# Performance work log

Measured on AMD Instinct MI355X. Metric: run time of the kernel, lower is better.

Reference implementation:

```python
import jax, jax.numpy as jnp
import numpy as np

N_QUBITS = 10
N_LAYERS = 4
DIM = 2 ** N_QUBITS  # 1024 statevector entries

# Z-expectation sign table: signs[d, q] = +1 if bit q of basis state d is 0 else -1
_bits = (np.arange(DIM)[:, None] >> (N_QUBITS - 1 - np.arange(N_QUBITS))) & 1
Z_SIGNS = jnp.asarray(1.0 - 2.0 * _bits, dtype=jnp.float32)  # [DIM, N_QUBITS]


def _apply_1q(state, mat, q):
    """Apply a 2x2 gate on qubit q. state: [B, DIM]; mat: [2,2] or [B,2,2]."""
    left, right = 2 ** q, 2 ** (N_QUBITS - q - 1)
    s = state.reshape(-1, left, 2, right)
    if mat.ndim == 3:
        s = jnp.einsum('bij,bljr->blir', mat, s)
    else:
        s = jnp.einsum('ij,bljr->blir', mat, s)
    return s.reshape(-1, DIM)


def _cnot_adj(state, q):
    """CNOT with control q, target q+1 (adjacent wires)."""
    left, right = 2 ** q, 2 ** (N_QUBITS - q - 2)
    s = state.reshape(-1, left, 2, 2, right)
    s = jnp.stack([s[:, :, 0], s[:, :, 1, ::-1]], axis=2)  # flip target where control=1
    return s.reshape(-1, DIM)


def _cnot_wrap(state):
    """CNOT with control = last qubit, target = qubit 0 (ring closure)."""
    s = state.reshape(-1, 2, 2 ** (N_QUBITS - 2), 2)  # [B, target, mid, control]
    s = jnp.stack([s[..., 0], s[:, ::-1, :, 1]], axis=-1)
    return s.reshape(-1, DIM)


def _circuit(x, weights):
    B = x.shape[0]
    state = jnp.zeros((B, DIM), jnp.complex64).at[:, 0].set(1.0)  # |0...0>

    # RX angle embedding (batch-dependent gates)
    c = jnp.cos(0.5 * x).astype(jnp.complex64)           # [B, n]
    s = (-1j) * jnp.sin(0.5 * x).astype(jnp.complex64)   # [B, n]
    for q in range(N_QUBITS):
        mat = jnp.stack([jnp.stack([c[:, q], s[:, q]], -1),
                         jnp.stack([s[:, q], c[:, q]], -1)], -2)  # [B,2,2]
        state = _apply_1q(state, mat, q)

    # BasicEntanglerLayers: per-qubit RY (shared weights) + CNOT ring
    w = weights.reshape(N_LAYERS, N_QUBITS)
    ch = jnp.cos(0.5 * w).astype(jnp.complex64)
    sh = jnp.sin(0.5 * w).astype(jnp.complex64)
    for l in range(N_LAYERS):
        for q in range(N_QUBITS):
            mat = jnp.stack([jnp.stack([ch[l, q], -sh[l, q]], -1),
                             jnp.stack([sh[l, q], ch[l, q]], -1)], -2)  # [2,2]
            state = _apply_1q(state, mat, q)
        for q in range(N_QUBITS - 1):
            state = _cnot_adj(state, q)
        state = _cnot_wrap(state)

    probs = state.real ** 2 + state.imag ** 2  # [B, DIM]
    return probs @ Z_SIGNS                     # [B, N_QUBITS] PauliZ expectations


def setup_inputs() -> dict:
    key = jax.random.key(0)
    k1, k2 = jax.random.split(key)
    x = jax.random.normal(k1, (2048, N_QUBITS), dtype=jnp.float32)
    weights = jax.random.normal(k2, (N_LAYERS * N_QUBITS,), dtype=jnp.float32)
    return {"x": x, "weights": weights}


def reference(x, weights):
    # Equivalent of: torch.stack([qnode(x[i], weights) for i in range(B)])
    # but fully batched over the statevector.
    return _circuit(x, weights)
```

## Files before the change

### kernel.cpp

```cpp
#include <hip/hip_runtime.h>

#define NQ 10
#define NL 4


template<int CTRL>
__device__ __forceinline__ float dppf(float v) {
    const int i = __float_as_int(v);
    const int r = __builtin_amdgcn_update_dpp(i, i, CTRL, 0xF, 0xF, false);
    return __int_as_float(r);
}
template<int OFF>
__device__ __forceinline__ float swzf(float v) {
    return __int_as_float(__builtin_amdgcn_ds_swizzle(__float_as_int(v), OFF));
}
__device__ __forceinline__ float bpermf(int addr4, float v) {
    return __int_as_float(__builtin_amdgcn_ds_bpermute(addr4, __float_as_int(v)));
}
__device__ __forceinline__ float rdlane(float v, int l) {
    return __int_as_float(__builtin_amdgcn_readlane(__float_as_int(v), l));
}

__global__ __launch_bounds__(256) void qnn_kernel(const float* __restrict__ x,
                                                  const float* __restrict__ w,
                                                  float* __restrict__ out,
                                                  int B) {
    const int lane = threadIdx.x & 63;
    const int b = blockIdx.x * 4 + (threadIdx.x >> 6);
    if (b >= B) return;

    float cxv = 1.f, sxv = 0.f, cwv = 1.f, swv = 0.f;
    if (lane < NQ) {
        const float a = 0.5f * x[b * NQ + lane];
        cxv = cosf(a); sxv = sinf(a);
    }
    if (lane < NL * NQ) {
        const float a = 0.5f * w[lane];
        cwv = cosf(a); swv = sinf(a);
    }

    float cq[NQ], sq[NQ];
#pragma unroll
    for (int q = 0; q < NQ; ++q) { cq[q] = rdlane(cxv, q); sq[q] = rdlane(sxv, q); }

    float ml = 1.f;
#pragma unroll
    for (int p = 0; p < 6; ++p) {
        ml *= ((lane >> p) & 1) ? sq[9 - p] : cq[9 - p];
    }
    const int kl = __popc(lane);
    const float cph = (kl & 1) ? 0.f : ((kl & 2) ? -1.f : 1.f);
    const float sph = (kl & 1) ? ((kl & 2) ? 1.f : -1.f) : 0.f;

    float m01[4], m23[4];
#pragma unroll
    for (int j = 0; j < 4; ++j) {
        m01[j] = ((j & 1) ? sq[3] : cq[3]) * ((j & 2) ? sq[2] : cq[2]);
        m23[j] = ((j & 1) ? sq[1] : cq[1]) * ((j & 2) ? sq[0] : cq[0]);
    }

    float2 v[16];
#pragma unroll
    for (int r = 0; r < 16; ++r) {
        const float M = ml * m01[r & 3] * m23[r >> 2];
        const int kr = ((r & 1) + ((r >> 1) & 1) + ((r >> 2) & 1) + ((r >> 3) & 1)) & 3;
        float re, im;
        if      (kr == 0) { re = cph;  im = sph;  }
        else if (kr == 1) { re = sph;  im = -cph; }
        else if (kr == 2) { re = -cph; im = -sph; }
        else              { re = -sph; im = cph;  }
        v[r] = make_float2(M * re, M * im);
    }

    int t = lane;
    t ^= ((t >> 1) & 1) << 0;
    t ^= ((t >> 2) & 1) << 1;
    t ^= ((t >> 3) & 1) << 2;
    t ^= ((t >> 4) & 1) << 3;
    t ^= ((t >> 5) & 1) << 4;
    const int ga4 = t << 2;
    const int gb4 = (t ^ 32) << 2;
    const int a32 = (lane ^ 32) << 2;
    const bool wrapctl = (lane & 1);

#pragma unroll
    for (int l = 0; l < NL; ++l) {
#pragma unroll
        for (int q = 0; q < 4; ++q) {
            const float c = rdlane(cwv, l * NQ + q);
            const float s = rdlane(swv, l * NQ + q);
            const int m = 1 << (3 - q);
#pragma unroll
            for (int r = 0; r < 16; ++r) {
                if (!(r & m)) {
                    const int r1 = r | m;
                    const float2 a0 = v[r], a1 = v[r1];
                    v[r]  = make_float2(c * a0.x - s * a1.x, c * a0.y - s * a1.y);
                    v[r1] = make_float2(s * a0.x + c * a1.x, s * a0.y + c * a1.y);
                }
            }
        }
        {
            const float c = rdlane(cwv, l * NQ + 4);
            const float s = rdlane(swv, l * NQ + 4);
            const float ss = (lane & 32) ? s : -s;
#pragma unroll
            for (int r = 0; r < 16; ++r) {
                const float ox = bpermf(a32, v[r].x);
                const float oy = bpermf(a32, v[r].y);
                v[r].x = fmaf(c, v[r].x, ss * ox);
                v[r].y = fmaf(c, v[r].y, ss * oy);
            }
        }
        {
            const float c = rdlane(cwv, l * NQ + 5);
            const float s = rdlane(swv, l * NQ + 5);
            const float ss = (lane & 16) ? s : -s;
#pragma unroll
            for (int r = 0; r < 16; ++r) {
                const float ox = swzf<0x401F>(v[r].x);
                const float oy = swzf<0x401F>(v[r].y);
                v[r].x = fmaf(c, v[r].x, ss * ox);
                v[r].y = fmaf(c, v[r].y, ss * oy);
            }
        }
        {
            const float c = rdlane(cwv, l * NQ + 6);
            const float s = rdlane(swv, l * NQ + 6);
            const float ss = (lane & 8) ? s : -s;
#pragma unroll
            for (int r = 0; r < 16; ++r) {
                const float ox = dppf<0x128>(v[r].x);
                const float oy = dppf<0x128>(v[r].y);
                v[r].x = fmaf(c, v[r].x, ss * ox);
                v[r].y = fmaf(c, v[r].y, ss * oy);
            }
        }
        {
            const float c = rdlane(cwv, l * NQ + 7);
            const float s = rdlane(swv, l * NQ + 7);
            const float ss = (lane & 4) ? s : -s;
#pragma unroll
            for (int r = 0; r < 16; ++r) {
                const float ox = swzf<0x101F>(v[r].x);
                const float oy = swzf<0x101F>(v[r].y);
                v[r].x = fmaf(c, v[r].x, ss * ox);
                v[r].y = fmaf(c, v[r].y, ss * oy);
            }
        }
        {
            const float c = rdlane(cwv, l * NQ + 8);
            const float s = rdlane(swv, l * NQ + 8);
            const float ss = (lane & 2) ? s : -s;
#pragma unroll
            for (int r = 0; r < 16; ++r) {
                const float ox = dppf<0x4E>(v[r].x);
                const float oy = dppf<0x4E>(v[r].y);
                v[r].x = fmaf(c, v[r].x, ss * ox);
                v[r].y = fmaf(c, v[r].y, ss * oy);
            }
        }
        {
            const float c = rdlane(cwv, l * NQ + 9);
            const float s = rdlane(swv, l * NQ + 9);
            const float ss = (lane & 1) ? s : -s;
#pragma unroll
            for (int r = 0; r < 16; ++r) {
                const float ox = dppf<0xB1>(v[r].x);
                const float oy = dppf<0xB1>(v[r].y);
                v[r].x = fmaf(c, v[r].x, ss * ox);
                v[r].y = fmaf(c, v[r].y, ss * oy);
            }
        }

        { float2 tmp;
          tmp = v[8];  v[8]  = v[12]; v[12] = tmp;
          tmp = v[9];  v[9]  = v[13]; v[13] = tmp;
          tmp = v[10]; v[10] = v[14]; v[14] = tmp;
          tmp = v[11]; v[11] = v[15]; v[15] = tmp; }
        { float2 tmp;
          tmp = v[4];  v[4]  = v[6];  v[6]  = tmp;
          tmp = v[5];  v[5]  = v[7];  v[7]  = tmp;
          tmp = v[12]; v[12] = v[14]; v[14] = tmp;
          tmp = v[13]; v[13] = v[15]; v[15] = tmp; }
        { float2 tmp;
          tmp = v[2];  v[2]  = v[3];  v[3]  = tmp;
          tmp = v[6];  v[6]  = v[7];  v[7]  = tmp;
          tmp = v[10]; v[10] = v[11]; v[11] = tmp;
          tmp = v[14]; v[14] = v[15]; v[15] = tmp; }
#pragma unroll
        for (int r = 0; r < 16; ++r) {
            const int a4 = (r & 1) ? gb4 : ga4;
            v[r].x = bpermf(a4, v[r].x);
            v[r].y = bpermf(a4, v[r].y);
        }
#pragma unroll
        for (int r = 0; r < 8; ++r) {
            const float2 a = v[r], c2 = v[r + 8];
            v[r]     = wrapctl ? c2 : a;
            v[r + 8] = wrapctl ? a : c2;
        }
    }

    float p[16];
    float T = 0.f;
#pragma unroll
    for (int r = 0; r < 16; ++r) {
        p[r] = v[r].x * v[r].x + v[r].y * v[r].y;
        T += p[r];
    }
    float S0 = 0.f, S1 = 0.f, S2 = 0.f, S3 = 0.f;
#pragma unroll
    for (int r = 0; r < 16; ++r) {
        S0 += (r & 8) ? -p[r] : p[r];
        S1 += (r & 4) ? -p[r] : p[r];
        S2 += (r & 2) ? -p[r] : p[r];
        S3 += (r & 1) ? -p[r] : p[r];
    }
    float acc[NQ];
    acc[0] = S0; acc[1] = S1; acc[2] = S2; acc[3] = S3;
#pragma unroll
    for (int q = 4; q < NQ; ++q) {
        acc[q] = ((lane >> (9 - q)) & 1) ? -T : T;
    }

#pragma unroll
    for (int q = 0; q < NQ; ++q) {
        float a = acc[q];
        a += bpermf(a32, a);
        a += swzf<0x401F>(a);
        a += dppf<0x128>(a);
        a += swzf<0x101F>(a);
        a += dppf<0x4E>(a);
        a += dppf<0xB1>(a);
        acc[q] = a;
    }
    if (lane == 0) {
#pragma unroll
        for (int q = 0; q < NQ; ++q) out[b * NQ + q] = acc[q];
    }
}

extern "C" void kernel_launch(void* const* d_in, const int* in_sizes, int n_in,
                              void* d_out, int out_size, void* d_ws, size_t ws_size,
                              hipStream_t stream) {
    const float* x = (const float*)d_in[0];
    const float* w = (const float*)d_in[1];
    float* out = (float*)d_out;
    const int B = in_sizes[0] / NQ;
    qnn_kernel<<<(B + 3) / 4, 256, 0, stream>>>(x, w, out, B);
}
```

Before: 71.47 us.

## Fold first entangler layer into product-state init and absorb final CNOT ring into readout

After: 66.75 us. 1.07x faster.

```diff
diff --git a/kernel.cpp b/kernel.cpp
--- a/kernel.cpp
+++ b/kernel.cpp
@@ -1,8 +1,9 @@
 #include <hip/hip_runtime.h>
 
 #define NQ 10
-#define NL 4
-
+
+
+typedef float v2f __attribute__((ext_vector_type(2)));
 
 template<int CTRL>
 __device__ __forceinline__ float dppf(float v) {
@@ -19,6 +20,13 @@
 }
 __device__ __forceinline__ float rdlane(float v, int l) {
     return __int_as_float(__builtin_amdgcn_readlane(__float_as_int(v), l));
+}
+__device__ __forceinline__ v2f splat(float a) { v2f r; r.x = a; r.y = a; return r; }
+__device__ __forceinline__ v2f cmul(v2f a, v2f b) {
+    v2f r;
+    r.x = a.x * b.x - a.y * b.y;
+    r.y = a.x * b.y + a.y * b.x;
+    return r;
 }
 
 __global__ __launch_bounds__(256) void qnn_kernel(const float* __restrict__ x,
@@ -34,43 +42,38 @@
         const float a = 0.5f * x[b * NQ + lane];
         cxv = cosf(a); sxv = sinf(a);
     }
-    if (lane < NL * NQ) {
+    if (lane < 4 * NQ) {
         const float a = 0.5f * w[lane];
         cwv = cosf(a); swv = sinf(a);
     }
 
-    float cq[NQ], sq[NQ];
-#pragma unroll
-    for (int q = 0; q < NQ; ++q) { cq[q] = rdlane(cxv, q); sq[q] = rdlane(sxv, q); }
-
-    float ml = 1.f;
-#pragma unroll
-    for (int p = 0; p < 6; ++p) {
-        ml *= ((lane >> p) & 1) ? sq[9 - p] : cq[9 - p];
-    }
-    const int kl = __popc(lane);
-    const float cph = (kl & 1) ? 0.f : ((kl & 2) ? -1.f : 1.f);
-    const float sph = (kl & 1) ? ((kl & 2) ? 1.f : -1.f) : 0.f;
-
-    float m01[4], m23[4];
+    v2f u0[NQ], u1[NQ];
+#pragma unroll
+    for (int q = 0; q < NQ; ++q) {
+        const float c  = rdlane(cxv, q), s  = rdlane(sxv, q);
+        const float ch = rdlane(cwv, q), sh = rdlane(swv, q);
+        u0[q].x = ch * c;  u0[q].y = sh * s;
+        u1[q].x = sh * c;  u1[q].y = -ch * s;
+    }
+
+    v2f ml = (lane & 1) ? u1[9] : u0[9];
+#pragma unroll
+    for (int p = 1; p < 6; ++p) {
+        const v2f f = ((lane >> p) & 1) ? u1[9 - p] : u0[9 - p];
+        ml = cmul(ml, f);
+    }
+    v2f m01[4], m23[4], tml[4];
 #pragma unroll
     for (int j = 0; j < 4; ++j) {
-        m01[j] = ((j & 1) ? sq[3] : cq[3]) * ((j & 2) ? sq[2] : cq[2]);
-        m23[j] = ((j & 1) ? sq[1] : cq[1]) * ((j & 2) ? sq[0] : cq[0]);
-    }
-
-    float2 v[16];
-#pragma unroll
-    for (int r = 0; r < 16; ++r) {
-        const float M = ml * m01[r & 3] * m23[r >> 2];
-        const int kr = ((r & 1) + ((r >> 1) & 1) + ((r >> 2) & 1) + ((r >> 3) & 1)) & 3;
-        float re, im;
-        if      (kr == 0) { re = cph;  im = sph;  }
-        else if (kr == 1) { re = sph;  im = -cph; }
-        else if (kr == 2) { re = -cph; im = -sph; }
-        else              { re = -sph; im = cph;  }
-        v[r] = make_float2(M * re, M * im);
-    }
+        m01[j] = cmul((j & 1) ? u1[3] : u0[3], (j & 2) ? u1[2] : u0[2]);
+        m23[j] = cmul((j & 1) ? u1[1] : u0[1], (j & 2) ? u1[0] : u0[0]);
+    }
+#pragma unroll
+    for (int j = 0; j < 4; ++j) tml[j] = cmul(ml, m01[j]);
+
+    v2f v[16];
+#pragma unroll
+    for (int r = 0; r < 16; ++r) v[r] = cmul(tml[r & 3], m23[r >> 2]);
 
     int t = lane;
     t ^= ((t >> 1) & 1) << 0;
@@ -84,106 +87,18 @@
     const bool wrapctl = (lane & 1);
 
 #pragma unroll
-    for (int l = 0; l < NL; ++l) {
-#pragma unroll
-        for (int q = 0; q < 4; ++q) {
-            const float c = rdlane(cwv, l * NQ + q);
-            const float s = rdlane(swv, l * NQ + q);
-            const int m = 1 << (3 - q);
-#pragma unroll
-            for (int r = 0; r < 16; ++r) {
-                if (!(r & m)) {
-                    const int r1 = r | m;
-                    const float2 a0 = v[r], a1 = v[r1];
-                    v[r]  = make_float2(c * a0.x - s * a1.x, c * a0.y - s * a1.y);
-                    v[r1] = make_float2(s * a0.x + c * a1.x, s * a0.y + c * a1.y);
-                }
-            }
-        }
-        {
-            const float c = rdlane(cwv, l * NQ + 4);
-            const float s = rdlane(swv, l * NQ + 4);
-            const float ss = (lane & 32) ? s : -s;
-#pragma unroll
-            for (int r = 0; r < 16; ++r) {
-                const float ox = bpermf(a32, v[r].x);
-                const float oy = bpermf(a32, v[r].y);
-                v[r].x = fmaf(c, v[r].x, ss * ox);
-                v[r].y = fmaf(c, v[r].y, ss * oy);
-            }
-        }
-        {
-            const float c = rdlane(cwv, l * NQ + 5);
-            const float s = rdlane(swv, l * NQ + 5);
-            const float ss = (lane & 16) ? s : -s;
-#pragma unroll
-            for (int r = 0; r < 16; ++r) {
-                const float ox = swzf<0x401F>(v[r].x);
-                const float oy = swzf<0x401F>(v[r].y);
-                v[r].x = fmaf(c, v[r].x, ss * ox);
-                v[r].y = fmaf(c, v[r].y, ss * oy);
-            }
-        }
-        {
-            const float c = rdlane(cwv, l * NQ + 6);
-            const float s = rdlane(swv, l * NQ + 6);
-            const float ss = (lane & 8) ? s : -s;
-#pragma unroll
-            for (int r = 0; r < 16; ++r) {
-                const float ox = dppf<0x128>(v[r].x);
-                const float oy = dppf<0x128>(v[r].y);
-                v[r].x = fmaf(c, v[r].x, ss * ox);
-                v[r].y = fmaf(c, v[r].y, ss * oy);
-            }
-        }
-        {
-            const float c = rdlane(cwv, l * NQ + 7);
-            const float s = rdlane(swv, l * NQ + 7);
-            const float ss = (lane & 4) ? s : -s;
-#pragma unroll
-            for (int r = 0; r < 16; ++r) {
-                const float ox = swzf<0x101F>(v[r].x);
-                const float oy = swzf<0x101F>(v[r].y);
-                v[r].x = fmaf(c, v[r].x, ss * ox);
-                v[r].y = fmaf(c, v[r].y, ss * oy);
-            }
-        }
-        {
-            const float c = rdlane(cwv, l * NQ + 8);
-            const float s = rdlane(swv, l * NQ + 8);
-            const float ss = (lane & 2) ? s : -s;
-#pragma unroll
-            for (int r = 0; r < 16; ++r) {
-                const float ox = dppf<0x4E>(v[r].x);
-                const float oy = dppf<0x4E>(v[r].y);
-                v[r].x = fmaf(c, v[r].x, ss * ox);
-                v[r].y = fmaf(c, v[r].y, ss * oy);
-            }
-        }
-        {
-            const float c = rdlane(cwv, l * NQ + 9);
-            const float s = rdlane(swv, l * NQ + 9);
-            const float ss = (lane & 1) ? s : -s;
-#pragma unroll
-            for (int r = 0; r < 16; ++r) {
-                const float ox = dppf<0xB1>(v[r].x);
-                const float oy = dppf<0xB1>(v[r].y);
-                v[r].x = fmaf(c, v[r].x, ss * ox);
-                v[r].y = fmaf(c, v[r].y, ss * oy);
-            }
-        }
-
-        { float2 tmp;
+    for (int l = 0; l < 3; ++l) {
+        { v2f tmp;
           tmp = v[8];  v[8]  = v[12]; v[12] = tmp;
           tmp = v[9];  v[9]  = v[13]; v[13] = tmp;
           tmp = v[10]; v[10] = v[14]; v[14] = tmp;
           tmp = v[11]; v[11] = v[15]; v[15] = tmp; }
-        { float2 tmp;
+        { v2f tmp;
           tmp = v[4];  v[4]  = v[6];  v[6]  = tmp;
           tmp = v[5];  v[5]  = v[7];  v[7]  = tmp;
           tmp = v[12]; v[12] = v[14]; v[14] = tmp;
           tmp = v[13]; v[13] = v[15]; v[15] = tmp; }
-        { float2 tmp;
+        { v2f tmp;
           tmp = v[2];  v[2]  = v[3];  v[3]  = tmp;
           tmp = v[6];  v[6]  = v[7];  v[7]  = tmp;
           tmp = v[10]; v[10] = v[11]; v[11] = tmp;
@@ -196,33 +111,121 @@
         }
 #pragma unroll
         for (int r = 0; r < 8; ++r) {
-            const float2 a = v[r], c2 = v[r + 8];
+            const v2f a = v[r], c2 = v[r + 8];
             v[r]     = wrapctl ? c2 : a;
             v[r + 8] = wrapctl ? a : c2;
         }
+
+        const int base = (l + 1) * NQ;
+#pragma unroll
+        for (int q = 0; q < 4; ++q) {
+            const v2f C = splat(rdlane(cwv, base + q));
+            const v2f S = splat(rdlane(swv, base + q));
+            const int m = 1 << (3 - q);
+#pragma unroll
+            for (int r = 0; r < 16; ++r) {
+                if (!(r & m)) {
+                    const int r1 = r | m;
+                    const v2f a0 = v[r], a1 = v[r1];
+                    v[r]  = C * a0 - S * a1;
+                    v[r1] = S * a0 + C * a1;
+                }
+            }
+        }
+        {
+            const float c = rdlane(cwv, base + 4);
+            const float s = rdlane(swv, base + 4);
+            const v2f C = splat(c);
+            const v2f SS = splat((lane & 32) ? s : -s);
+#pragma unroll
+            for (int r = 0; r < 16; ++r) {
+                v2f o; o.x = bpermf(a32, v[r].x); o.y = bpermf(a32, v[r].y);
+                v[r] = C * v[r] + SS * o;
+            }
+        }
+        {
+            const float c = rdlane(cwv, base + 5);
+            const float s = rdlane(swv, base + 5);
+            const v2f C = splat(c);
+            const v2f SS = splat((lane & 16) ? s : -s);
+#pragma unroll
+            for (int r = 0; r < 16; ++r) {
+                v2f o; o.x = swzf<0x401F>(v[r].x); o.y = swzf<0x401F>(v[r].y);
+                v[r] = C * v[r] + SS * o;
+            }
+        }
+        {
+            const float c = rdlane(cwv, base + 6);
+            const float s = rdlane(swv, base + 6);
+            const v2f C = splat(c);
+            const v2f SS = splat((lane & 8) ? s : -s);
+#pragma unroll
+            for (int r = 0; r < 16; ++r) {
+                v2f o; o.x = dppf<0x128>(v[r].x); o.y = dppf<0x128>(v[r].y);
+                v[r] = C * v[r] + SS * o;
+            }
+        }
+        {
+            const float c = rdlane(cwv, base + 7);
+            const float s = rdlane(swv, base + 7);
+            const v2f C = splat(c);
+            const v2f SS = splat((lane & 4) ? s : -s);
+#pragma unroll
+            for (int r = 0; r < 16; ++r) {
+                v2f o; o.x = swzf<0x101F>(v[r].x); o.y = swzf<0x101F>(v[r].y);
+                v[r] = C * v[r] + SS * o;
+            }
+        }
+        {
+            const float c = rdlane(cwv, base + 8);
+            const float s = rdlane(swv, base + 8);
+            const v2f C = splat(c);
+            const v2f SS = splat((lane & 2) ? s : -s);
+#pragma unroll
+            for (int r = 0; r < 16; ++r) {
+                v2f o; o.x = dppf<0x4E>(v[r].x); o.y = dppf<0x4E>(v[r].y);
+                v[r] = C * v[r] + SS * o;
+            }
+        }
+        {
+            const float c = rdlane(cwv, base + 9);
+            const float s = rdlane(swv, base + 9);
+            const v2f C = splat(c);
+            const v2f SS = splat((lane & 1) ? s : -s);
+#pragma unroll
+            for (int r = 0; r < 16; ++r) {
+                v2f o; o.x = dppf<0xB1>(v[r].x); o.y = dppf<0xB1>(v[r].y);
+                v[r] = C * v[r] + SS * o;
+            }
+        }
     }
 
     float p[16];
-    float T = 0.f;
+#pragma unroll
+    for (int r = 0; r < 16; ++r) p[r] = v[r].x * v[r].x + v[r].y * v[r].y;
+
+    float S15 = 0.f, S7 = 0.f, S12 = 0.f, S14 = 0.f;
 #pragma unroll
     for (int r = 0; r < 16; ++r) {
-        p[r] = v[r].x * v[r].x + v[r].y * v[r].y;
-        T += p[r];
-    }
-    float S0 = 0.f, S1 = 0.f, S2 = 0.f, S3 = 0.f;
-#pragma unroll
-    for (int r = 0; r < 16; ++r) {
-        S0 += (r & 8) ? -p[r] : p[r];
-        S1 += (r & 4) ? -p[r] : p[r];
-        S2 += (r & 2) ? -p[r] : p[r];
-        S3 += (r & 1) ? -p[r] : p[r];
-    }
+        const float pr = p[r];
+        S15 += (__popc(r) & 1)      ? -pr : pr;
+        S7  += (__popc(r & 7) & 1)  ? -pr : pr;
+        S12 += (__popc(r & 12) & 1) ? -pr : pr;
+        S14 += (__popc(r & 14) & 1) ? -pr : pr;
+    }
+
+    const float gAll = (__popc(lane) & 1) ? -1.f : 1.f;
     float acc[NQ];
-    acc[0] = S0; acc[1] = S1; acc[2] = S2; acc[3] = S3;
-#pragma unroll
-    for (int q = 4; q < NQ; ++q) {
-        acc[q] = ((lane >> (9 - q)) & 1) ? -T : T;
-    }
+    acc[0] = gAll * S7;
+    acc[1] = S12;
+    acc[2] = S14;
+    acc[3] = S15;
+    acc[4] = ((lane >> 5) & 1) ? -S15 : S15;
+    acc[5] = (__popc(lane & 0x30) & 1) ? -S15 : S15;
+    acc[6] = (__popc(lane & 0x38) & 1) ? -S15 : S15;
+    acc[7] = (__popc(lane & 0x3C) & 1) ? -S15 : S15;
+    acc[8] = (__popc(lane & 0x3E) & 1) ? -S15 : S15;
+    acc[9] = gAll * S15;
 
 #pragma unroll
     for (int q = 0; q < NQ; ++q) {
```
